# Kernel tuning notes

Hardware: AMD Instinct MI355X
Metric: run time of the kernel (lower is better)

## Reference

```python
import jax, jax.numpy as jnp
import numpy as np

D_MODEL = 1024
N_HEADS = 16
D_K = D_MODEL // N_HEADS
B, S = 4, 2048
NEG = -1e9


def setup_inputs() -> dict:
    key = jax.random.key(0)
    ks = jax.random.split(key, 9)
    scale = 1.0 / np.sqrt(D_MODEL)
    x = jax.random.normal(ks[0], (B, S, D_MODEL), dtype=jnp.float32)
    mask = jnp.tril(jnp.ones((S, S), dtype=jnp.int32))  # causal lower-triangular
    Wq = jax.random.normal(ks[1], (D_MODEL, D_MODEL), dtype=jnp.float32) * scale
    Wk = jax.random.normal(ks[2], (D_MODEL, D_MODEL), dtype=jnp.float32) * scale
    Wv = jax.random.normal(ks[3], (D_MODEL, D_MODEL), dtype=jnp.float32) * scale
    Wo = jax.random.normal(ks[4], (D_MODEL, D_MODEL), dtype=jnp.float32) * scale
    bq = jnp.zeros((D_MODEL,), dtype=jnp.float32)
    bk = jnp.zeros((D_MODEL,), dtype=jnp.float32)
    bv = jnp.zeros((D_MODEL,), dtype=jnp.float32)
    bo = jnp.zeros((D_MODEL,), dtype=jnp.float32)
    return {"x": x, "mask": mask, "Wq": Wq, "bq": bq, "Wk": Wk, "bk": bk,
            "Wv": Wv, "bv": bv, "Wo": Wo, "bo": bo}


def reference(x, mask, Wq, bq, Wk, bk, Wv, bv, Wo, bo):
    b, s, _ = x.shape
    # nn.Linear: y = x @ W.T + b
    Q = x @ Wq.T + bq
    K = x @ Wk.T + bk
    V = x @ Wv.T + bv
    # [b, h, s, d_k]
    Q = Q.reshape(b, s, N_HEADS, D_K).transpose(0, 2, 1, 3)
    K = K.reshape(b, s, N_HEADS, D_K).transpose(0, 2, 1, 3)
    V = V.reshape(b, s, N_HEADS, D_K).transpose(0, 2, 1, 3)
    score = jnp.einsum('bhqd,bhkd->bhqk', Q, K) / jnp.sqrt(jnp.float32(D_K))
    score = jnp.where(mask == 0, jnp.float32(NEG), score)
    attn = jax.nn.softmax(score, axis=-1)
    out = jnp.einsum('bhqk,bhkd->bhqd', attn, V)
    out = out.transpose(0, 2, 1, 3).reshape(b, s, D_MODEL)
    return out @ Wo.T + bo
```

## Files before the change

### kernel.cpp

```cpp
#include <hip/hip_runtime.h>
#include <hip/hip_bf16.h>
#include <stdint.h>

typedef __bf16 bf16x8 __attribute__((ext_vector_type(8)));
typedef float  f32x4  __attribute__((ext_vector_type(4)));

#define B_   4
#define S_   2048
#define DM   1024
#define H_   16
#define DK   64
#define M_TOT 8192

__device__ __forceinline__ void gld16(const __bf16* g, char* l) {
    __builtin_amdgcn_global_load_lds(
        (const __attribute__((address_space(1))) void*)g,
        (__attribute__((address_space(3))) void*)l,
        16, 0, 0);
}

__global__ __launch_bounds__(256)
void cvt_f32_bf16(const float* __restrict__ in, __bf16* __restrict__ out, int n) {
    int i = (blockIdx.x * 256 + threadIdx.x) * 8;
    if (i >= n) return;
    float4 a = *(const float4*)(in + i);
    float4 c = *(const float4*)(in + i + 4);
    bf16x8 o;
    o[0] = (__bf16)a.x; o[1] = (__bf16)a.y; o[2] = (__bf16)a.z; o[3] = (__bf16)a.w;
    o[4] = (__bf16)c.x; o[5] = (__bf16)c.y; o[6] = (__bf16)c.z; o[7] = (__bf16)c.w;
    *(bf16x8*)(out + i) = o;
}

__global__ __launch_bounds__(256)
void cvt4_w(const float* __restrict__ w0, const float* __restrict__ w1,
            const float* __restrict__ w2, const float* __restrict__ w3,
            __bf16* __restrict__ out) {
    const int z = blockIdx.z;
    const float* in = (z == 0) ? w0 : (z == 1) ? w1 : (z == 2) ? w2 : w3;
    int i = (blockIdx.x * 256 + threadIdx.x) * 8;
    float4 a = *(const float4*)(in + i);
    float4 c = *(const float4*)(in + i + 4);
    bf16x8 o;
    o[0] = (__bf16)a.x; o[1] = (__bf16)a.y; o[2] = (__bf16)a.z; o[3] = (__bf16)a.w;
    o[4] = (__bf16)c.x; o[5] = (__bf16)c.y; o[6] = (__bf16)c.z; o[7] = (__bf16)c.w;
    *(bf16x8*)(out + (size_t)z * (DM * DM) + i) = o;
}

__device__ __forceinline__ void gemm_core(const __bf16* __restrict__ A,
                                          const __bf16* __restrict__ W,
                                          int m0, int n0,
                                          f32x4 (&acc)[4][4]) {
    __shared__ __bf16 As[128 * 32];
    __shared__ __bf16 Bs[128 * 32];
    const int tid  = threadIdx.x;
    const int wid  = tid >> 6;
    const int lane = tid & 63;
    const int ln15 = lane & 15, lg = lane >> 4;
    const int wr = (wid >> 1) * 64;
    const int wc = (wid & 1) * 64;

    const int c1 = tid, c2 = tid + 256;
    const int ar1 = m0 + (c1 >> 2), ac1 = (c1 & 3) * 8;
    const int ar2 = m0 + (c2 >> 2), ac2 = (c2 & 3) * 8;
    const int br1 = n0 + (c1 >> 2);
    const int br2 = n0 + (c2 >> 2);
    char* la1 = (char*)As + wid * 1024;
    char* la2 = la1 + 4096;
    char* lb1 = (char*)Bs + wid * 1024;
    char* lb2 = lb1 + 4096;

    for (int k0 = 0; k0 < DM; k0 += 32) {
        gld16(A + (size_t)ar1 * DM + k0 + ac1, la1);
        gld16(A + (size_t)ar2 * DM + k0 + ac2, la2);
        gld16(W + (size_t)br1 * DM + k0 + ac1, lb1);
        gld16(W + (size_t)br2 * DM + k0 + ac2, lb2);
        __syncthreads();
        bf16x8 af[4], bfr[4];
#pragma unroll
        for (int m = 0; m < 4; ++m)
            af[m] = *(const bf16x8*)&As[(wr + m * 16 + ln15) * 32 + lg * 8];
#pragma unroll
        for (int n = 0; n < 4; ++n)
            bfr[n] = *(const bf16x8*)&Bs[(wc + n * 16 + ln15) * 32 + lg * 8];
#pragma unroll
        for (int m = 0; m < 4; ++m)
#pragma unroll
            for (int n = 0; n < 4; ++n)
                acc[m][n] = __builtin_amdgcn_mfma_f32_16x16x32_bf16(af[m], bfr[n], acc[m][n], 0, 0, 0);
        __syncthreads();
    }
}

__global__ __launch_bounds__(256)
void gemm_qkv_kernel(const __bf16* __restrict__ Xb,
                     const __bf16* __restrict__ Wq, const __bf16* __restrict__ Wk,
                     const __bf16* __restrict__ Wv,
                     const float* __restrict__ bq, const float* __restrict__ bk,
                     const float* __restrict__ bv,
                     __bf16* __restrict__ Qb, __bf16* __restrict__ Kb,
                     __bf16* __restrict__ Vt) {
    const int z = blockIdx.z;
    const __bf16* W   = (z == 0) ? Wq : (z == 1) ? Wk : Wv;
    const float* bias = (z == 0) ? bq : (z == 1) ? bk : bv;
    const int m0 = blockIdx.x * 128, n0 = blockIdx.y * 128;

    f32x4 acc[4][4] = {};
    gemm_core(Xb, W, m0, n0, acc);

    const int tid = threadIdx.x, wid = tid >> 6, lane = tid & 63;
    const int ln15 = lane & 15, lg = lane >> 4;
    const int wr = (wid >> 1) * 64, wc = (wid & 1) * 64;
    const float oscl = (z == 0) ? 0.18033688f : 1.0f;

    if (z < 2) {
        __bf16* out = (z == 0) ? Qb : Kb;
#pragma unroll
        for (int ni = 0; ni < 4; ++ni) {
            int col = n0 + wc + ni * 16 + ln15;
            int h = col >> 6, d = col & 63;
            float bval = bias[col];
#pragma unroll
            for (int mi = 0; mi < 4; ++mi)
#pragma unroll
                for (int r = 0; r < 4; ++r) {
                    int row = m0 + wr + mi * 16 + lg * 4 + r;
                    int b = row >> 11, s = row & 2047;
                    out[(((size_t)(b * H_ + h)) * S_ + s) * DK + d] =
                        (__bf16)((acc[mi][ni][r] + bval) * oscl);
                }
        }
    } else {
#pragma unroll
        for (int ni = 0; ni < 4; ++ni) {
            int col = n0 + wc + ni * 16 + ln15;
            int h = col >> 6, d = col & 63;
            float bval = bias[col];
#pragma unroll
            for (int mi = 0; mi < 4; ++mi)
#pragma unroll
                for (int r = 0; r < 4; ++r) {
                    int row = m0 + wr + mi * 16 + lg * 4 + r;
                    int b = row >> 11, s = row & 2047;
                    Vt[(((size_t)(b * H_ + h)) * DK + d) * S_ + s] =
                        (__bf16)(acc[mi][ni][r] + bval);
                }
        }
    }
}

__global__ __launch_bounds__(256)
void gemm_out_kernel(const __bf16* __restrict__ Ab, const __bf16* __restrict__ Wo,
                     const float* __restrict__ bo, float* __restrict__ out) {
    const int m0 = blockIdx.x * 128, n0 = blockIdx.y * 128;
    f32x4 acc[4][4] = {};
    gemm_core(Ab, Wo, m0, n0, acc);

    const int tid = threadIdx.x, wid = tid >> 6, lane = tid & 63;
    const int ln15 = lane & 15, lg = lane >> 4;
    const int wr = (wid >> 1) * 64, wc = (wid & 1) * 64;
#pragma unroll
    for (int ni = 0; ni < 4; ++ni) {
        int col = n0 + wc + ni * 16 + ln15;
        float bval = bo[col];
#pragma unroll
        for (int mi = 0; mi < 4; ++mi)
#pragma unroll
            for (int r = 0; r < 4; ++r) {
                int row = m0 + wr + mi * 16 + lg * 4 + r;
                out[(size_t)row * DM + col] = acc[mi][ni][r] + bval;
            }
    }
}

__global__ __launch_bounds__(512)
void attn_kernel(const __bf16* __restrict__ Qb, const __bf16* __restrict__ Kb,
                 const __bf16* __restrict__ Vt, __bf16* __restrict__ AO) {
    __shared__ __bf16 Ks[2][128 * 64];
    __shared__ __bf16 Vs[2][64 * 128];

    const int tid = threadIdx.x, wid = tid >> 6, lane = tid & 63;
    const int ln15 = lane & 15, lg = lane >> 4;
    const int bh = blockIdx.y;
    const size_t base = (size_t)bh * (S_ * DK);
    const int b = bh >> 4, h = bh & 15;

    const int krow = wid * 8 + (lane >> 3);
    const int kswz = ((lane & 7) ^ (krow & 7)) * 8;
    const int vrow = wid * 4 + (lane >> 4);
    const int vswz = ((lane & 15) ^ (vrow & 7)) * 8;
    const int swz  = (ln15 & 7) << 3;

    const __bf16* kgb = Kb + base;
    const __bf16* vgb = Vt + base;

    auto stage = [&](int buf, int kt) {
        char* dk = (char*)Ks + buf * 16384 + wid * 1024;
        char* dv = (char*)Vs + buf * 16384 + wid * 1024;
        gld16(kgb + (size_t)(kt * 128 + krow) * DK + kswz, dk);
        gld16(kgb + (size_t)(kt * 128 + krow + 64) * DK + kswz, dk + 8192);
        gld16(vgb + (size_t)vrow * S_ + kt * 128 + vswz, dv);
        gld16(vgb + (size_t)(vrow + 32) * S_ + kt * 128 + vswz, dv + 8192);
    };

    bf16x8 ones;
#pragma unroll
    for (int j = 0; j < 8; ++j) ones[j] = (__bf16)1.0f;

#pragma unroll
    for (int ph = 0; ph < 2; ++ph) {
        const int qb   = ph ? (int)blockIdx.x : 15 - (int)blockIdx.x;
        const int last = qb;
        const int qr0  = qb * 128 + wid * 16 + ln15;

        bf16x8 qf[2];
        {
            int q0 = qr0;
            qf[0] = *(const bf16x8*)&Qb[base + (size_t)q0 * DK + lg * 8];
            qf[1] = *(const bf16x8*)&Qb[base + (size_t)q0 * DK + 32 + lg * 8];
        }

        f32x4 acc[4] = {};
        f32x4 lacc = {};

        __builtin_amdgcn_s_barrier();
        stage(0, 0);
        asm volatile("s_waitcnt vmcnt(0)" ::: "memory");
        __builtin_amdgcn_s_barrier();
        __builtin_amdgcn_sched_barrier(0);

        for (int kt = 0; kt <= last; ++kt) {
            const int cur = kt & 1;
            if (kt < last) stage(cur ^ 1, kt + 1);

            const __bf16* ksb = &Ks[cur][0];
            const __bf16* vsb = &Vs[cur][0];

            f32x4 z[8] = {};
            __builtin_amdgcn_s_setprio(1);
#pragma unroll
            for (int cb = 0; cb < 8; ++cb)
#pragma unroll
                for (int kk = 0; kk < 2; ++kk) {
                    bf16x8 kf = *(const bf16x8*)&ksb[(cb * 16 + ln15) * 64 + ((kk * 32 + lg * 8) ^ swz)];
                    z[cb] = __builtin_amdgcn_mfma_f32_16x16x32_bf16(kf, qf[kk], z[cb], 0, 0, 0);
                }
            __builtin_amdgcn_s_setprio(0);

            if (kt == last) {
                const int kcb = kt * 128 + lg * 4;
#pragma unroll
                for (int cb = 0; cb < 8; ++cb)
#pragma unroll
                    for (int r = 0; r < 4; ++r)
                        if (kcb + cb * 16 + r > qr0) z[cb][r] = -3e8f;
            }

            uint32_t a0[8], b0[8];
#pragma unroll
            for (int cb = 0; cb < 8; ++cb) {
                float e0 = exp2f(z[cb][0]), e1 = exp2f(z[cb][1]);
                float e2 = exp2f(z[cb][2]), e3 = exp2f(z[cb][3]);
                asm("v_cvt_pk_bf16_f32 %0, %1, %2" : "=v"(a0[cb]) : "v"(e0), "v"(e1));
                asm("v_cvt_pk_bf16_f32 %0, %1, %2" : "=v"(b0[cb]) : "v"(e2), "v"(e3));
            }

            union U8 { uint32_t u[4]; bf16x8 v; };
            bf16x8 pa[4];
#pragma unroll
            for (int ks = 0; ks < 4; ++ks) {
                uint32_t x = a0[2 * ks], y = a0[2 * ks + 1];
                asm("v_permlane32_swap_b32 %0, %1" : "+v"(x), "+v"(y));
                asm("v_permlane16_swap_b32 %0, %1" : "+v"(x), "+v"(y));
                uint32_t p = b0[2 * ks], q = b0[2 * ks + 1];
                asm("v_permlane32_swap_b32 %0, %1" : "+v"(p), "+v"(q));
                asm("v_permlane16_swap_b32 %0, %1" : "+v"(p), "+v"(q));
                U8 f; f.u[0] = x; f.u[1] = p; f.u[2] = y; f.u[3] = q;
                pa[ks] = f.v;
            }

            __builtin_amdgcn_s_setprio(1);
#pragma unroll
            for (int ks = 0; ks < 4; ++ks) {
                lacc = __builtin_amdgcn_mfma_f32_16x16x32_bf16(pa[ks], ones, lacc, 0, 0, 0);
#pragma unroll
                for (int db = 0; db < 4; ++db) {
                    bf16x8 vf = *(const bf16x8*)&vsb[(db * 16 + ln15) * 128 + ((ks * 32 + lg * 8) ^ swz)];
                    acc[db] = __builtin_amdgcn_mfma_f32_16x16x32_bf16(pa[ks], vf, acc[db], 0, 0, 0);
                }
            }
            __builtin_amdgcn_s_setprio(0);

            if (kt < last) {
                asm volatile("s_waitcnt vmcnt(0)" ::: "memory");
                __builtin_amdgcn_s_barrier();
                __builtin_amdgcn_sched_barrier(0);
            }
        }

#pragma unroll
        for (int r = 0; r < 4; ++r) {
            float i0 = 1.f / lacc[r];
            int s0r = qb * 128 + wid * 16 + lg * 4 + r;
#pragma unroll
            for (int db = 0; db < 4; ++db)
                AO[((size_t)(b * S_ + s0r)) * DM + h * DK + db * 16 + ln15] = (__bf16)(acc[db][r] * i0);
        }
    }
}

extern "C" void kernel_launch(void* const* d_in, const int* in_sizes, int n_in,
                              void* d_out, int out_size, void* d_ws, size_t ws_size,
                              hipStream_t stream) {
    const float* x  = (const float*)d_in[0];
    const float* Wq = (const float*)d_in[2];
    const float* bq = (const float*)d_in[3];
    const float* Wk = (const float*)d_in[4];
    const float* bk = (const float*)d_in[5];
    const float* Wv = (const float*)d_in[6];
    const float* bv = (const float*)d_in[7];
    const float* Wo = (const float*)d_in[8];
    const float* bo = (const float*)d_in[9];
    float* out = (float*)d_out;

    char* ws = (char*)d_ws;
    __bf16* xb  = (__bf16*)ws;
    __bf16* wqb = (__bf16*)(ws + 16777216);
    __bf16* wkb = wqb + 1048576;
    __bf16* wvb = wkb + 1048576;
    __bf16* wob = wvb + 1048576;
    __bf16* Qb  = (__bf16*)(ws + 25165824);
    __bf16* Kb  = Qb + 8388608;
    __bf16* Vt  = Kb + 8388608;
    __bf16* AO  = xb;

    cvt_f32_bf16<<<4096, 256, 0, stream>>>(x, xb, M_TOT * DM);
    cvt4_w<<<dim3(512, 1, 4), 256, 0, stream>>>(Wq, Wk, Wv, Wo, wqb);

    gemm_qkv_kernel<<<dim3(64, 8, 3), 256, 0, stream>>>(xb, wqb, wkb, wvb,
                                                        bq, bk, bv, Qb, Kb, Vt);
    attn_kernel<<<dim3(8, 64), 512, 0, stream>>>(Qb, Kb, Vt, AO);
    gemm_out_kernel<<<dim3(64, 8), 256, 0, stream>>>(AO, wob, bo, out);
}
```

Measured before the change: 187.4 us.

## Double-buffer LDS tiles in GEMM core to overlap global loads with MFMA

The shared GEMM core now keeps two LDS buffers for the A and W tiles and issues the async global-to-LDS loads for the next K step before computing on the current one. One explicit vmcnt wait and barrier per iteration replaces the two syncthreads. The goal is to hide global load latency behind the MFMA work in the QKV and output projections. It doubles LDS use per block, which may lower occupancy. The single barrier per step relies on the LDS reads being complete before the next overwrite, which is only safe if the compiler orders them ahead of the barrier.

```diff
diff --git a/kernel.cpp b/kernel.cpp
--- a/kernel.cpp
+++ b/kernel.cpp
@@ -50,8 +50,8 @@
                                           const __bf16* __restrict__ W,
                                           int m0, int n0,
                                           f32x4 (&acc)[4][4]) {
-    __shared__ __bf16 As[128 * 32];
-    __shared__ __bf16 Bs[128 * 32];
+    __shared__ __bf16 As[2][128 * 32];
+    __shared__ __bf16 Bs[2][128 * 32];
     const int tid  = threadIdx.x;
     const int wid  = tid >> 6;
     const int lane = tid & 63;
@@ -64,30 +64,45 @@
     const int ar2 = m0 + (c2 >> 2), ac2 = (c2 & 3) * 8;
     const int br1 = n0 + (c1 >> 2);
     const int br2 = n0 + (c2 >> 2);
-    char* la1 = (char*)As + wid * 1024;
-    char* la2 = la1 + 4096;
-    char* lb1 = (char*)Bs + wid * 1024;
-    char* lb2 = lb1 + 4096;
-
-    for (int k0 = 0; k0 < DM; k0 += 32) {
-        gld16(A + (size_t)ar1 * DM + k0 + ac1, la1);
-        gld16(A + (size_t)ar2 * DM + k0 + ac2, la2);
-        gld16(W + (size_t)br1 * DM + k0 + ac1, lb1);
-        gld16(W + (size_t)br2 * DM + k0 + ac2, lb2);
-        __syncthreads();
+
+    auto stage = [&](int buf, int k0) {
+        char* la = (char*)&As[buf][0] + wid * 1024;
+        char* lb = (char*)&Bs[buf][0] + wid * 1024;
+        gld16(A + (size_t)ar1 * DM + k0 + ac1, la);
+        gld16(A + (size_t)ar2 * DM + k0 + ac2, la + 4096);
+        gld16(W + (size_t)br1 * DM + k0 + ac1, lb);
+        gld16(W + (size_t)br2 * DM + k0 + ac2, lb + 4096);
+    };
+
+    stage(0, 0);
+    asm volatile("s_waitcnt vmcnt(0)" ::: "memory");
+    __builtin_amdgcn_s_barrier();
+    __builtin_amdgcn_sched_barrier(0);
+
+    for (int t = 0; t < 32; ++t) {
+        const int cur = t & 1;
+        if (t < 31) stage(cur ^ 1, (t + 1) * 32);
+
+        const __bf16* as = &As[cur][0];
+        const __bf16* bs = &Bs[cur][0];
         bf16x8 af[4], bfr[4];
 #pragma unroll
         for (int m = 0; m < 4; ++m)
-            af[m] = *(const bf16x8*)&As[(wr + m * 16 + ln15) * 32 + lg * 8];
+            af[m] = *(const bf16x8*)&as[(wr + m * 16 + ln15) * 32 + lg * 8];
 #pragma unroll
         for (int n = 0; n < 4; ++n)
-            bfr[n] = *(const bf16x8*)&Bs[(wc + n * 16 + ln15) * 32 + lg * 8];
+            bfr[n] = *(const bf16x8*)&bs[(wc + n * 16 + ln15) * 32 + lg * 8];
 #pragma unroll
         for (int m = 0; m < 4; ++m)
 #pragma unroll
             for (int n = 0; n < 4; ++n)
                 acc[m][n] = __builtin_amdgcn_mfma_f32_16x16x32_bf16(af[m], bfr[n], acc[m][n], 0, 0, 0);
-        __syncthreads();
+
+        if (t < 31) {
+            asm volatile("s_waitcnt vmcnt(0)" ::: "memory");
+            __builtin_amdgcn_s_barrier();
+            __builtin_amdgcn_sched_barrier(0);
+        }
     }
 }
 
```

Result: slower. 204.4 us (+9.1%).
